# Kernel optimization log

Measured on AMD Instinct MI355X. Metric: run time of the kernel, lower is better.

Reference implementation:

```python
import jax, jax.numpy as jnp
import numpy as np

B, N = 2, 4096
SA, DG, ED, OUT = 128, 1024, 4, 128
RF = 0.1   # ED_radius_factor
EPS = 1e-5  # BatchNorm eps


def setup_inputs() -> dict:
    key = jax.random.key(0)
    ks = jax.random.split(key, 16)
    def w(k, sh, sc=0.05):
        return jax.random.normal(k, sh, jnp.float32) * sc
    return dict(
        pointcloud=jax.random.normal(ks[0], (B, N, 3), jnp.float32),
        h1=jax.random.normal(ks[1], (B, SA, N), jnp.float32),
        h2=jax.random.normal(ks[2], (B, DG, N), jnp.float32),
        dg_w1=w(ks[3], (256, DG)), dg_b1=jnp.zeros(256), dg_g1=jnp.ones(256), dg_be1=jnp.zeros(256),
        dg_w2=w(ks[4], (64, 256)), dg_b2=jnp.zeros(64), dg_g2=jnp.ones(64), dg_be2=jnp.zeros(64),
        dg_w3=w(ks[5], (32, 64)), dg_b3=jnp.zeros(32), dg_g3=jnp.ones(32), dg_be3=jnp.zeros(32),
        ed_w1=w(ks[6], (3, ED), 0.5), ed_b1=jnp.zeros(ED),
        ed_w2=w(ks[7], (ED, ED), 0.5), ed_b2=jnp.zeros(ED),
        w1=w(ks[8], (512, SA + 32 + ED)), b1=jnp.zeros(512), g1=jnp.ones(512), be1=jnp.zeros(512),
        w2=w(ks[9], (256, 512)), b2=jnp.zeros(256), g2=jnp.ones(256), be2=jnp.zeros(256),
        w3=w(ks[10], (OUT, 256)), b3=jnp.zeros(OUT), g3=jnp.ones(OUT), be3=jnp.zeros(OUT),
    )


def _conv1x1(x, w, b):  # x: (B,C,N) 1x1 Conv1d
    return jnp.einsum('oc,bcn->bon', w, x) + b[None, :, None]


def _bn(x, g, b):  # training-mode BatchNorm1d over (B,N) per channel
    m = x.mean(axis=(0, 2), keepdims=True)
    v = ((x - m) ** 2).mean(axis=(0, 2), keepdims=True)
    return g[None, :, None] * (x - m) * jax.lax.rsqrt(v + EPS) + b[None, :, None]


def _eigs(xyz):  # (N,3) -> (N,3) eigenvalues of per-point radius-neighbor covariance
    n = xyz.shape[0]
    x2 = (xyz * xyz).sum(-1)
    d2 = jnp.maximum(x2[:, None] + x2[None, :] - 2.0 * (xyz @ xyz.T), 0.0)
    dist = jnp.sqrt(jnp.maximum(d2, 1e-12))
    eye = jnp.eye(n, dtype=bool)
    max_d = jnp.where(eye, -jnp.inf, dist).max()  # calculate_distances max
    radius = max_d * RF                            # adaptive radius
    mask = ((dist < radius) & ~eye).astype(xyz.dtype)  # (N,N) radius neighbors, no self
    cnt = mask.sum(1)                              # true neighbor count (for the mean)
    mu = (mask @ xyz) / jnp.maximum(cnt, 1.0)[:, None]
    # sum_j m_ij x_j x_j^T via one matmul on flattened outer products
    S = (mask @ (xyz[:, :, None] * xyz[:, None, :]).reshape(n, 9)).reshape(n, 3, 3)
    # NOTE: original divides by k = mask.shape[0] == N (not neighbor count) -- kept faithfully
    cov = (S - cnt[:, None, None] * mu[:, :, None] * mu[:, None, :]) / n
    return jnp.linalg.eigvalsh(cov)


def reference(pointcloud, h1, h2,
              dg_w1, dg_b1, dg_g1, dg_be1,
              dg_w2, dg_b2, dg_g2, dg_be2,
              dg_w3, dg_b3, dg_g3, dg_be3,
              ed_w1, ed_b1, ed_w2, ed_b2,
              w1, b1, g1, be1, w2, b2, g2, be2, w3, b3, g3, be3):
    xyz = pointcloud[..., 0:3]
    # DG head: 1024 -> 256 -> 64 -> 32 (1x1 conv + BN + ReLU)
    f2 = jax.nn.relu(_bn(_conv1x1(h2, dg_w1, dg_b1), dg_g1, dg_be1))
    f2 = jax.nn.relu(_bn(_conv1x1(f2, dg_w2, dg_b2), dg_g2, dg_be2))
    f2 = jax.nn.relu(_bn(_conv1x1(f2, dg_w3, dg_b3), dg_g3, dg_be3))
    # ED branch: per-point local PCA eigenvalues + tiny MLP (3->4->4)
    eig = jax.vmap(_eigs)(xyz)                        # (B,N,3)
    h3 = jax.nn.relu(eig @ ed_w1 + ed_b1) @ ed_w2 + ed_b2  # (B,N,4)
    z = jnp.concatenate([h1, f2, jnp.transpose(h3, (0, 2, 1))], axis=1)  # (B,164,N)
    z = jax.nn.relu(_bn(_conv1x1(z, w1, b1), g1, be1))
    z = jax.nn.relu(_bn(_conv1x1(z, w2, b2), g2, be2))
    z = jax.nn.relu(_bn(_conv1x1(z, w3, b3), g3, be3))
    return (xyz, z)
```

## Files before the change

### kernel.cpp

```cpp
#include <hip/hip_runtime.h>
#include <math.h>

#define NPTS 4096
#define NB 2
#define BIGNEG -3.0e38f

typedef __attribute__((ext_vector_type(8))) short short8;
typedef __attribute__((ext_vector_type(4))) float f32x4;
typedef unsigned int uint32;

__device__ __forceinline__ unsigned short f2bf(float f) {
  uint32 u = __float_as_uint(f);
  uint32 r = (u + 0x7FFFu + ((u >> 16) & 1u)) >> 16;
  return (unsigned short)r;
}
__device__ __forceinline__ uint2 pack4(float a, float b, float c, float d) {
  uint2 r;
  r.x = (uint32)f2bf(a) | ((uint32)f2bf(b) << 16);
  r.y = (uint32)f2bf(c) | ((uint32)f2bf(d) << 16);
  return r;
}
__device__ __forceinline__ uint32 packtr(float lo, float hi) {
  return __builtin_amdgcn_perm(__float_as_uint(hi), __float_as_uint(lo), 0x07060302u);
}
__device__ __forceinline__ float bflo(uint32 w) { return __uint_as_float((w & 0xffffu) << 16); }
__device__ __forceinline__ float bfhi(uint32 w) { return __uint_as_float(w & 0xffff0000u); }

struct PrepP {
  const float *h2, *h1, *pc;
  const float* wsrc[6];
  unsigned short* wdst[6];
  unsigned short *h2t, *Zt;
  float *aZ, *bZ, *fZ, *f0;
  unsigned int* mx;
};

union ShPrep {
  float tile[64][65];
  struct { float4 sp[512]; float lm[8]; } m;
};

__global__ __launch_bounds__(256)
void prep_maxd2(PrepP P) {
  __shared__ ShPrep sh;
  int bid = blockIdx.x, tid = threadIdx.x;
  if (bid < 2304) {
    const float* src; unsigned short* dst; int S, C, b, c0, n0;
    if (bid < 2048) {
      b = bid >> 10; int r = bid & 1023;
      c0 = (r & 15) * 64; n0 = (r >> 4) * 64;
      src = P.h2; dst = P.h2t; S = 1024; C = 1024;
    } else {
      int r = bid - 2048; b = r >> 7; int r2 = r & 127;
      c0 = (r2 & 1) * 64; n0 = (r2 >> 1) * 64;
      src = P.h1; dst = P.Zt; S = 192; C = 128;
    }
    const float* sb = src + (size_t)b * C * NPTS;
#pragma unroll
    for (int p = 0; p < 4; ++p) {
      int r = (tid >> 4) + p * 16, q = tid & 15;
      float4 v = *(const float4*)(sb + (size_t)(c0 + r) * NPTS + n0 + q * 4);
      sh.tile[r][q * 4 + 0] = v.x;
      sh.tile[r][q * 4 + 1] = v.y;
      sh.tile[r][q * 4 + 2] = v.z;
      sh.tile[r][q * 4 + 3] = v.w;
    }
    __syncthreads();
#pragma unroll
    for (int p = 0; p < 2; ++p) {
      int n = (tid >> 3) + p * 32, j = tid & 7;
      uint2 lo = pack4(sh.tile[j * 8 + 0][n], sh.tile[j * 8 + 1][n], sh.tile[j * 8 + 2][n],
                       sh.tile[j * 8 + 3][n]);
      uint2 hi = pack4(sh.tile[j * 8 + 4][n], sh.tile[j * 8 + 5][n], sh.tile[j * 8 + 6][n],
                       sh.tile[j * 8 + 7][n]);
      *(uint4*)(dst + ((size_t)b * NPTS + n0 + n) * S + c0 + j * 8) =
          make_uint4(lo.x, lo.y, hi.x, hi.y);
    }
  } else if (bid < 2336) {
    int r = bid - 2304;
    for (int idx = r * 256 + tid; idx < NB * NPTS * 7; idx += 32 * 256) {
      int u = idx % 7, n = (idx / 7) & (NPTS - 1), b = idx / (7 * NPTS);
      *(uint2*)(P.Zt + ((size_t)b * NPTS + n) * 192 + 164 + u * 4) = make_uint2(0u, 0u);
    }
  } else if (bid < 2592) {
    const int segKp[6] = {1024, 256, 64, 192, 512, 256};
    const int segM[6] = {256, 64, 32, 512, 256, 128};
    const int segK[6] = {1024, 256, 64, 164, 512, 256};
    const int segEnd[6] = {262144, 278528, 282624, 380928, 512000, 544768};
    int r = bid - 2336;
    for (int idx = r * 256 + tid; idx < 544768; idx += 256 * 256) {
      int w = 0, start = 0;
#pragma unroll
      for (int s = 0; s < 6; ++s)
        if (idx >= segEnd[s]) { w = s + 1; start = segEnd[s]; }
      int local = idx - start, Kp = segKp[w], m = local / Kp, k = local % Kp;
      float v = (m < segM[w] && k < segK[w]) ? P.wsrc[w][m * segK[w] + k] : 0.f;
      P.wdst[w][local] = f2bf(v);
    }
  } else if (bid == 2592) {
    for (int ch = tid; ch < 512; ch += 256) {
      P.f0[ch] = 0.f;
      if (ch < 192) { P.aZ[ch] = 1.f; P.bZ[ch] = 0.f; P.fZ[ch] = BIGNEG; }
    }
  } else {
    int vb = bid - 2593;
    int b = vb >> 9, rem = vb & 511, it = rem & 63, jt = rem >> 6;
    int i0 = it * 64, j0 = jt * 512;
    const float* pb = P.pc + (size_t)b * NPTS * 3;
    for (int t = tid; t < 512; t += 256) {
      int j = j0 + t;
      float x = pb[j * 3], y = pb[j * 3 + 1], z = pb[j * 3 + 2];
      sh.m.sp[t] = make_float4(x, y, z, fmaf(x, x, fmaf(y, y, z * z)));
    }
    __syncthreads();
    int il = tid & 63, sl = tid >> 6;
    int i = i0 + il;
    float xi = pb[i * 3], yi = pb[i * 3 + 1], zi = pb[i * 3 + 2];
    float x2i = fmaf(xi, xi, fmaf(yi, yi, zi * zi));
    float m = 0.f;
#pragma unroll 4
    for (int j = sl * 128, e2 = sl * 128 + 128; j < e2; ++j) {
      float4 pj = sh.m.sp[j];
      float dot = fmaf(xi, pj.x, fmaf(yi, pj.y, zi * pj.z));
      m = fmaxf(m, fmaf(-2.f, dot, x2i + pj.w));
    }
#pragma unroll
    for (int off = 32; off > 0; off >>= 1) m = fmaxf(m, __shfl_xor(m, off, 64));
    if ((tid & 63) == 0) sh.m.lm[tid >> 6] = m;
    __syncthreads();
    if (tid == 0) {
      float v = fmaxf(fmaxf(sh.m.lm[0], sh.m.lm[1]), fmaxf(sh.m.lm[2], sh.m.lm[3]));
      atomicMax(&P.mx[b], __float_as_uint(v));
    }
  }
}

struct GemmP {
  const unsigned short* Wp;
  const unsigned short* X;
  const float *aIn, *bIn, *fIn;
  unsigned short* Y;
  int Ystride;
  float *psum, *psq;
  int M, Kp;
};
struct EigP {
  const float* pc;
  const unsigned int* mx;
  float* part;
  const float *ew1, *eb1, *ew2, *eb2;
  unsigned short* Zt;
};

union ShG {
  struct { char db[2][18432]; float ash[512], bsh[512], fsh[512]; } g;
  struct { float4 sp[1024]; float red[4][32][10]; } e;
};

template <int BN_IN, int EIG>
__global__ __launch_bounds__(256)
void gemm_k(GemmP P, EigP E) {
  __shared__ ShG sh;
  const int tid = threadIdx.x;

  if (EIG == 1 && blockIdx.z >= NB) {
    int e = blockIdx.x + 32 * blockIdx.y + 128 * (blockIdx.z - NB);
    int b = e >> 9, rem = e & 511, it = rem & 127, js = rem >> 7;
    int i0 = it * 32, j0 = js * 1024;
    const float* pb = E.pc + (size_t)b * NPTS * 3;
    for (int t = tid; t < 1024; t += 256) {
      int j = j0 + t;
      float x = pb[j * 3], y = pb[j * 3 + 1], z = pb[j * 3 + 2];
      sh.e.sp[t] = make_float4(x, y, z, fmaf(x, x, fmaf(y, y, z * z)));
    }
    __syncthreads();
    int il = tid & 31, sl = tid >> 5;
    int i = i0 + il;
    float xi = pb[i * 3], yi = pb[i * 3 + 1], zi = pb[i * 3 + 2];
    float x2i = fmaf(xi, xi, fmaf(yi, yi, zi * zi));
    float r2 = 0.01f * fmaxf(__uint_as_float(E.mx[b]), 1e-12f);
    float v0 = 0, v1 = 0, v2 = 0, v3 = 0, v4 = 0, v5 = 0, v6 = 0, v7 = 0, v8 = 0, v9 = 0;
#pragma unroll 2
    for (int j = sl * 128, e2 = sl * 128 + 128; j < e2; ++j) {
      float4 pj = sh.e.sp[j];
      float dot = fmaf(xi, pj.x, fmaf(yi, pj.y, zi * pj.z));
      float d2 = fmaf(-2.f, dot, x2i + pj.w);
      float msk = d2 < r2 ? 1.f : 0.f;
      float qx = msk * pj.x, qy = msk * pj.y, qz = msk * pj.z;
      v0 += msk; v1 += qx; v2 += qy; v3 += qz;
      v4 = fmaf(qx, pj.x, v4); v5 = fmaf(qx, pj.y, v5); v6 = fmaf(qx, pj.z, v6);
      v7 = fmaf(qy, pj.y, v7); v8 = fmaf(qy, pj.z, v8); v9 = fmaf(qz, pj.z, v9);
    }
    int iloc = i - j0;
    if (iloc >= sl * 128 && iloc < sl * 128 + 128) {
      v0 -= 1.f; v1 -= xi; v2 -= yi; v3 -= zi;
      v4 = fmaf(-xi, xi, v4); v5 = fmaf(-xi, yi, v5); v6 = fmaf(-xi, zi, v6);
      v7 = fmaf(-yi, yi, v7); v8 = fmaf(-yi, zi, v8); v9 = fmaf(-zi, zi, v9);
    }
    float vals[10] = {v0, v1, v2, v3, v4, v5, v6, v7, v8, v9};
#pragma unroll
    for (int v = 0; v < 10; ++v) vals[v] += __shfl_xor(vals[v], 32, 64);
    int w = tid >> 6;
    if ((tid & 63) < 32)
#pragma unroll
      for (int v = 0; v < 10; ++v) sh.e.red[w][il][v] = vals[v];
    __syncthreads();
    if (tid < 32) {
      int ii = i0 + tid;
      size_t base = ((size_t)(b * 4 + js) * 10) * NPTS + ii;
#pragma unroll
      for (int v = 0; v < 10; ++v)
        E.part[base + (size_t)v * NPTS] =
            sh.e.red[0][tid][v] + sh.e.red[1][tid][v] + sh.e.red[2][tid][v] +
            sh.e.red[3][tid][v];
    }
    return;
  }

  if (EIG == 2 && blockIdx.z >= NB) {
    int p = blockIdx.x * 256 + tid;
    int b = p >> 12, i = p & (NPTS - 1);
    float t[10];
#pragma unroll
    for (int v = 0; v < 10; ++v) {
      float s = 0.f;
#pragma unroll
      for (int js = 0; js < 4; ++js)
        s += E.part[((size_t)(b * 4 + js) * 10 + v) * NPTS + i];
      t[v] = s;
    }
    double cntd = (double)t[0];
    double denom = cntd > 1.0 ? cntd : 1.0;
    double mux = t[1] / denom, muy = t[2] / denom, muz = t[3] / denom;
    const double inv_n = 1.0 / (double)NPTS;
    double a00 = ((double)t[4] - cntd * mux * mux) * inv_n;
    double a01 = ((double)t[5] - cntd * mux * muy) * inv_n;
    double a02 = ((double)t[6] - cntd * mux * muz) * inv_n;
    double a11 = ((double)t[7] - cntd * muy * muy) * inv_n;
    double a12 = ((double)t[8] - cntd * muy * muz) * inv_n;
    double a22 = ((double)t[9] - cntd * muz * muz) * inv_n;
    double e0, e1, e2;
    double p1 = a01 * a01 + a02 * a02 + a12 * a12;
    double q = (a00 + a11 + a22) / 3.0;
    double d0 = a00 - q, d1 = a11 - q, d2q = a22 - q;
    double p2 = d0 * d0 + d1 * d1 + d2q * d2q + 2.0 * p1;
    if (p2 <= 1e-30) {
      e0 = e1 = e2 = q;
    } else {
      double pp = sqrt(p2 / 6.0);
      double ip = 1.0 / pp;
      double b00 = d0 * ip, b11 = d1 * ip, b22 = d2q * ip;
      double b01 = a01 * ip, b02 = a02 * ip, b12 = a12 * ip;
      double detB = b00 * (b11 * b22 - b12 * b12) - b01 * (b01 * b22 - b12 * b02) +
                    b02 * (b01 * b12 - b11 * b02);
      double r = detB * 0.5;
      r = r < -1.0 ? -1.0 : (r > 1.0 ? 1.0 : r);
      double phi = acos(r) / 3.0;
      e2 = q + 2.0 * pp * cos(phi);
      e0 = q + 2.0 * pp * cos(phi + 2.0943951023931953);
      e1 = 3.0 * q - e0 - e2;
    }
    float eg[3] = {(float)e0, (float)e1, (float)e2};
    float tmp[4];
#pragma unroll
    for (int e = 0; e < 4; ++e) {
      float v = E.eb1[e];
#pragma unroll
      for (int k = 0; k < 3; ++k) v = fmaf(eg[k], E.ew1[k * 4 + e], v);
      tmp[e] = fmaxf(v, 0.f);
    }
    float h3[4];
#pragma unroll
    for (int f = 0; f < 4; ++f) {
      float v = E.eb2[f];
#pragma unroll
      for (int e = 0; e < 4; ++e) v = fmaf(tmp[e], E.ew2[e * 4 + f], v);
      h3[f] = v;
    }
    *(uint2*)(E.Zt + ((size_t)b * NPTS + i) * 192 + 160) = pack4(h3[0], h3[1], h3[2], h3[3]);
    return;
  }

  const int b = blockIdx.z, nt = blockIdx.x, mt = blockIdx.y;
  const int n0 = nt * 128, m0 = mt * 64;
  const int lane = tid & 63, wid = tid >> 6;
  const int wm = wid >> 1, wn = wid & 1, g = lane >> 4, c = lane & 15;
  const int kt = P.Kp >> 6;
  const unsigned short* Xb = P.X + (size_t)b * NPTS * P.Kp;

  if (BN_IN) {
    for (int ch = tid; ch < P.Kp; ch += 256) {
      sh.g.ash[ch] = P.aIn[ch];
      sh.g.bsh[ch] = P.bIn[ch];
      sh.g.fsh[ch] = P.fIn[ch];
    }
    __syncthreads();
  }

  uint4 R0[4], R1[4];
  auto loadG = [&](int t, uint4* R) {
    int k0 = t << 6;
#pragma unroll
    for (int i = 0; i < 4; ++i) {
      int u = tid + i * 256, n = u >> 3, s = u & 7;
      R[i] = *(const uint4*)(Xb + (size_t)(n0 + n) * P.Kp + k0 + s * 8);
    }
  };
  auto writeS = [&](int buf, int t, uint4* R) {
    int k0 = t << 6;
#pragma unroll
    for (int i = 0; i < 4; ++i) {
      int u = tid + i * 256, s = u & 7;
      uint4 v = R[i];
      if (BN_IN) {
        int k = k0 + s * 8;
        float4 a0 = *(const float4*)&sh.g.ash[k], a1 = *(const float4*)&sh.g.ash[k + 4];
        float4 b0 = *(const float4*)&sh.g.bsh[k], b1 = *(const float4*)&sh.g.bsh[k + 4];
        float4 f0 = *(const float4*)&sh.g.fsh[k], f1 = *(const float4*)&sh.g.fsh[k + 4];
        float e0 = fmaxf(fmaf(bflo(v.x), a0.x, b0.x), f0.x);
        float e1 = fmaxf(fmaf(bfhi(v.x), a0.y, b0.y), f0.y);
        float e2 = fmaxf(fmaf(bflo(v.y), a0.z, b0.z), f0.z);
        float e3 = fmaxf(fmaf(bfhi(v.y), a0.w, b0.w), f0.w);
        float e4 = fmaxf(fmaf(bflo(v.z), a1.x, b1.x), f1.x);
        float e5 = fmaxf(fmaf(bfhi(v.z), a1.y, b1.y), f1.y);
        float e6 = fmaxf(fmaf(bflo(v.w), a1.z, b1.z), f1.z);
        float e7 = fmaxf(fmaf(bfhi(v.w), a1.w, b1.w), f1.w);
        v.x = packtr(e0, e1);
        v.y = packtr(e2, e3);
        v.z = packtr(e4, e5);
        v.w = packtr(e6, e7);
      }
      *(uint4*)&sh.g.db[buf][(u >> 3) * 144 + (u & 7) * 16] = v;
    }
  };
  auto loadA = [&](int t, uint4* Af) {
    const unsigned short* base = P.Wp + (size_t)(m0 + wm * 32 + c) * P.Kp + (t << 6) + g * 8;
#pragma unroll
    for (int mf = 0; mf < 2; ++mf)
#pragma unroll
      for (int kw = 0; kw < 2; ++kw)
        Af[mf * 2 + kw] = *(const uint4*)(base + (size_t)mf * 16 * P.Kp + kw * 32);
  };

  f32x4 acc[2][4] = {};
  uint4 Acur[4], Anext[4] = {};
  loadG(0, R0);
  loadA(0, Acur);
  writeS(0, 0, R0);
  if (kt > 1) loadG(1, R1);
  __syncthreads();
  int cur = 0;

  auto step = [&](int t, uint4* Rload, uint4* Rwrite) {
    if (t + 2 < kt) loadG(t + 2, Rload);
    if (t + 1 < kt) loadA(t + 1, Anext);
#pragma unroll
    for (int kw = 0; kw < 2; ++kw) {
      union { uint4 u; short8 s; } a0, a1;
      a0.u = Acur[0 * 2 + kw];
      a1.u = Acur[1 * 2 + kw];
#pragma unroll
      for (int nf = 0; nf < 4; ++nf) {
        union { uint4 u; short8 s; } bf;
        bf.u = *(const uint4*)&sh.g.db[cur][(wn * 64 + nf * 16 + c) * 144 + kw * 64 + g * 16];
        acc[0][nf] = __builtin_amdgcn_mfma_f32_16x16x32_bf16(a0.s, bf.s, acc[0][nf], 0, 0, 0);
        acc[1][nf] = __builtin_amdgcn_mfma_f32_16x16x32_bf16(a1.s, bf.s, acc[1][nf], 0, 0, 0);
      }
    }
    if (t + 1 < kt) writeS(cur ^ 1, t + 1, Rwrite);
    __syncthreads();
    cur ^= 1;
#pragma unroll
    for (int i = 0; i < 4; ++i) Acur[i] = Anext[i];
  };
  for (int t = 0; t < kt;) {
    step(t, R0, R1);
    ++t;
    if (t >= kt) break;
    step(t, R1, R0);
    ++t;
  }

#pragma unroll
  for (int nf = 0; nf < 4; ++nf) {
    int n = n0 + wn * 64 + nf * 16 + c;
    unsigned short* yrow = P.Y + ((size_t)b * NPTS + n) * P.Ystride;
#pragma unroll
    for (int mf = 0; mf < 2; ++mf) {
      int mb = m0 + wm * 32 + mf * 16 + g * 4;
      if (mb < P.M)
        *(uint2*)(yrow + mb) =
            pack4(acc[mf][nf][0], acc[mf][nf][1], acc[mf][nf][2], acc[mf][nf][3]);
    }
  }
  int slot = b * 64 + nt * 2 + wn;
#pragma unroll
  for (int mf = 0; mf < 2; ++mf)
#pragma unroll
    for (int r = 0; r < 4; ++r) {
      float s = 0.f, q = 0.f;
#pragma unroll
      for (int nf = 0; nf < 4; ++nf) {
        float v = acc[mf][nf][r];
        s += v;
        q = fmaf(v, v, q);
      }
#pragma unroll
      for (int m = 1; m < 16; m <<= 1) {
        s += __shfl_xor(s, m, 64);
        q += __shfl_xor(q, m, 64);
      }
      int row = m0 + wm * 32 + mf * 16 + g * 4 + r;
      if (c == 0 && row < P.M) {
        P.psum[(size_t)row * 128 + slot] = s;
        P.psq[(size_t)row * 128 + slot] = q;
      }
    }
}

__global__ __launch_bounds__(128)
void bn_finalize(const float* __restrict__ psum, const float* __restrict__ psq,
                 const float* __restrict__ gamma, const float* __restrict__ beta,
                 float* __restrict__ a_, float* __restrict__ b_, float* __restrict__ f_) {
  int ch = blockIdx.x, t = threadIdx.x;
  float s = psum[(size_t)ch * 128 + t];
  float q = psq[(size_t)ch * 128 + t];
#pragma unroll
  for (int m = 1; m < 64; m <<= 1) {
    s += __shfl_xor(s, m, 64);
    q += __shfl_xor(q, m, 64);
  }
  __shared__ float ws[2][2];
  if ((t & 63) == 0) { ws[t >> 6][0] = s; ws[t >> 6][1] = q; }
  __syncthreads();
  if (t == 0) {
    float S = ws[0][0] + ws[1][0];
    float Q = ws[0][1] + ws[1][1];
    const float inv = 1.f / (float)(NB * NPTS);
    float mean = S * inv;
    float var = fmaxf(Q * inv - mean * mean, 0.f);
    float aa = rsqrtf(var + 1e-5f) * gamma[ch];
    a_[ch] = aa;
    b_[ch] = beta[ch] - mean * aa;
    if (f_) f_[ch] = 0.f;
  }
}

__global__ __launch_bounds__(256)
void out_final(const unsigned short* __restrict__ Y, const float* __restrict__ a_,
               const float* __restrict__ b_, const float* __restrict__ pc,
               float* __restrict__ out) {
  int bid = blockIdx.x;
  if (bid < 1024) {
    __shared__ float tile[32][33];
    int b = bid >> 9, r0 = bid & 511;
    int c0 = (r0 & 3) * 32, n0 = (r0 >> 2) * 32;
    int r = threadIdx.x >> 3, q = threadIdx.x & 7;
    uint2 v = *(const uint2*)(Y + ((size_t)b * NPTS + n0 + r) * 128 + c0 + q * 4);
    float4 aa = *(const float4*)(a_ + c0 + q * 4);
    float4 bb = *(const float4*)(b_ + c0 + q * 4);
    tile[r][q * 4 + 0] = fmaxf(bflo(v.x) * aa.x + bb.x, 0.f);
    tile[r][q * 4 + 1] = fmaxf(bfhi(v.x) * aa.y + bb.y, 0.f);
    tile[r][q * 4 + 2] = fmaxf(bflo(v.y) * aa.z + bb.z, 0.f);
    tile[r][q * 4 + 3] = fmaxf(bfhi(v.y) * aa.w + bb.w, 0.f);
    __syncthreads();
    float4 o = make_float4(tile[q * 4 + 0][r], tile[q * 4 + 1][r], tile[q * 4 + 2][r],
                           tile[q * 4 + 3][r]);
    float* z = out + (size_t)NB * NPTS * 3;
    *(float4*)(z + ((size_t)b * 128 + c0 + r) * NPTS + n0 + q * 4) = o;
  } else {
    int i = (bid - 1024) * 256 + threadIdx.x;
    ((float4*)out)[i] = ((const float4*)pc)[i];
  }
}

extern "C" void kernel_launch(void* const* d_in, const int* in_sizes, int n_in,
                              void* d_out, int out_size, void* d_ws, size_t ws_size,
                              hipStream_t stream) {
  (void)in_sizes; (void)n_in; (void)out_size; (void)ws_size;
  const float* pc    = (const float*)d_in[0];
  const float* h1    = (const float*)d_in[1];
  const float* h2    = (const float*)d_in[2];
  const float* dgw1  = (const float*)d_in[3];
  const float* dgg1  = (const float*)d_in[5];
  const float* dgbe1 = (const float*)d_in[6];
  const float* dgw2  = (const float*)d_in[7];
  const float* dgg2  = (const float*)d_in[9];
  const float* dgbe2 = (const float*)d_in[10];
  const float* dgw3  = (const float*)d_in[11];
  const float* dgg3  = (const float*)d_in[13];
  const float* dgbe3 = (const float*)d_in[14];
  const float* ew1   = (const float*)d_in[15];
  const float* eb1   = (const float*)d_in[16];
  const float* ew2   = (const float*)d_in[17];
  const float* eb2   = (const float*)d_in[18];
  const float* w1    = (const float*)d_in[19];
  const float* g1    = (const float*)d_in[21];
  const float* be1   = (const float*)d_in[22];
  const float* w2    = (const float*)d_in[23];
  const float* g2    = (const float*)d_in[25];
  const float* be2   = (const float*)d_in[26];
  const float* w3    = (const float*)d_in[27];
  const float* g3    = (const float*)d_in[29];
  const float* be3   = (const float*)d_in[30];
  float* out = (float*)d_out;

  char* p = (char*)d_ws;
  auto take = [&](size_t bytes) { char* r = p; p += (bytes + 255) & ~(size_t)255; return r; };
  unsigned int* mx = (unsigned int*)take(64);
  unsigned short* h2t = (unsigned short*)take((size_t)NB * NPTS * 1024 * 2);
  unsigned short* Zt  = (unsigned short*)take((size_t)NB * NPTS * 192 * 2);
  unsigned short* wp1 = (unsigned short*)take((size_t)256 * 1024 * 2);
  unsigned short* wp2 = (unsigned short*)take((size_t)64 * 256 * 2);
  unsigned short* wp3 = (unsigned short*)take((size_t)64 * 64 * 2);
  unsigned short* wp4 = (unsigned short*)take((size_t)512 * 192 * 2);
  unsigned short* wp5 = (unsigned short*)take((size_t)256 * 512 * 2);
  unsigned short* wp6 = (unsigned short*)take((size_t)128 * 256 * 2);
  unsigned short* yA  = (unsigned short*)take((size_t)NB * NPTS * 256 * 2);
  unsigned short* yB  = (unsigned short*)take((size_t)NB * NPTS * 512 * 2);
  float* psum = (float*)take((size_t)512 * 128 * 4);
  float* psq  = (float*)take((size_t)512 * 128 * 4);
  float* a1 = (float*)take(512 * 4); float* b1 = (float*)take(512 * 4);
  float* a2 = (float*)take(512 * 4); float* b2 = (float*)take(512 * 4);
  float* aZ = (float*)take(512 * 4); float* bZ = (float*)take(512 * 4);
  float* fZ = (float*)take(512 * 4);
  float* a4 = (float*)take(512 * 4); float* b4 = (float*)take(512 * 4);
  float* a5 = (float*)take(512 * 4); float* b5 = (float*)take(512 * 4);
  float* a6 = (float*)take(512 * 4); float* b6 = (float*)take(512 * 4);
  float* f0 = (float*)take(512 * 4);
  float* part = (float*)take((size_t)NB * 4 * 10 * NPTS * 4);

  hipMemsetAsync(mx, 0, 64, stream);

  PrepP PP;
  PP.h2 = h2; PP.h1 = h1; PP.pc = pc;
  PP.wsrc[0] = dgw1; PP.wsrc[1] = dgw2; PP.wsrc[2] = dgw3;
  PP.wsrc[3] = w1;   PP.wsrc[4] = w2;   PP.wsrc[5] = w3;
  PP.wdst[0] = wp1; PP.wdst[1] = wp2; PP.wdst[2] = wp3;
  PP.wdst[3] = wp4; PP.wdst[4] = wp5; PP.wdst[5] = wp6;
  PP.h2t = h2t; PP.Zt = Zt;
  PP.aZ = aZ; PP.bZ = bZ; PP.fZ = fZ; PP.f0 = f0;
  PP.mx = mx;
  prep_maxd2<<<3617, 256, 0, stream>>>(PP);

  EigP EP = {pc, mx, part, ew1, eb1, ew2, eb2, Zt};

  GemmP L1 = {wp1, h2t, nullptr, nullptr, nullptr, yA, 256, psum, psq, 256, 1024};
  gemm_k<0, 1><<<dim3(32, 4, NB + 8), 256, 0, stream>>>(L1, EP);
  bn_finalize<<<256, 128, 0, stream>>>(psum, psq, dgg1, dgbe1, a1, b1, nullptr);

  GemmP L2 = {wp2, yA, a1, b1, f0, yB, 64, psum, psq, 64, 256};
  gemm_k<1, 2><<<dim3(32, 1, NB + 1), 256, 0, stream>>>(L2, EP);
  bn_finalize<<<64, 128, 0, stream>>>(psum, psq, dgg2, dgbe2, a2, b2, nullptr);

  GemmP L3 = {wp3, yB, a2, b2, f0, Zt + 128, 192, psum, psq, 32, 64};
  gemm_k<1, 0><<<dim3(32, 1, NB), 256, 0, stream>>>(L3, EP);
  bn_finalize<<<32, 128, 0, stream>>>(psum, psq, dgg3, dgbe3, aZ + 128, bZ + 128, fZ + 128);

  GemmP L4 = {wp4, Zt, aZ, bZ, fZ, yB, 512, psum, psq, 512, 192};
  gemm_k<1, 0><<<dim3(32, 8, NB), 256, 0, stream>>>(L4, EP);
  bn_finalize<<<512, 128, 0, stream>>>(psum, psq, g1, be1, a4, b4, nullptr);

  GemmP L5 = {wp5, yB, a4, b4, f0, yA, 256, psum, psq, 256, 512};
  gemm_k<1, 0><<<dim3(32, 4, NB), 256, 0, stream>>>(L5, EP);
  bn_finalize<<<256, 128, 0, stream>>>(psum, psq, g2, be2, a5, b5, nullptr);

  GemmP L6 = {wp6, yA, a5, b5, f0, yB, 128, psum, psq, 128, 256};
  gemm_k<1, 0><<<dim3(32, 2, NB), 256, 0, stream>>>(L6, EP);
  bn_finalize<<<128, 128, 0, stream>>>(psum, psq, g3, be3, a6, b6, nullptr);

  out_final<<<1048, 256, 0, stream>>>(yB, a6, b6, pc, out);
}
```

Baseline: 140.5 us.

## Fuse BatchNorm finalize into the prologue of each following GEMM

```diff
diff --git a/kernel.cpp b/kernel.cpp
--- a/kernel.cpp
+++ b/kernel.cpp
@@ -31,7 +31,6 @@
   const float* wsrc[6];
   unsigned short* wdst[6];
   unsigned short *h2t, *Zt;
-  float *aZ, *bZ, *fZ, *f0;
   unsigned int* mx;
 };
 
@@ -97,13 +96,8 @@
       float v = (m < segM[w] && k < segK[w]) ? P.wsrc[w][m * segK[w] + k] : 0.f;
       P.wdst[w][local] = f2bf(v);
     }
-  } else if (bid == 2592) {
-    for (int ch = tid; ch < 512; ch += 256) {
-      P.f0[ch] = 0.f;
-      if (ch < 192) { P.aZ[ch] = 1.f; P.bZ[ch] = 0.f; P.fZ[ch] = BIGNEG; }
-    }
   } else {
-    int vb = bid - 2593;
+    int vb = bid - 2592;
     int b = vb >> 9, rem = vb & 511, it = rem & 63, jt = rem >> 6;
     int i0 = it * 64, j0 = jt * 512;
     const float* pb = P.pc + (size_t)b * NPTS * 3;
@@ -138,10 +132,11 @@
 struct GemmP {
   const unsigned short* Wp;
   const unsigned short* X;
-  const float *aIn, *bIn, *fIn;
+  const float *psIn, *pqIn, *gam, *bet;
+  int chOff, nch;
   unsigned short* Y;
   int Ystride;
-  float *psum, *psq;
+  float *psO, *pqO;
   int M, Kp;
 };
 struct EigP {
@@ -290,9 +285,30 @@
 
   if (BN_IN) {
     for (int ch = tid; ch < P.Kp; ch += 256) {
-      sh.g.ash[ch] = P.aIn[ch];
-      sh.g.bsh[ch] = P.bIn[ch];
-      sh.g.fsh[ch] = P.fIn[ch];
+      sh.g.ash[ch] = 1.f;
+      sh.g.bsh[ch] = 0.f;
+      sh.g.fsh[ch] = BIGNEG;
+    }
+    __syncthreads();
+    for (int idx = tid; idx < P.nch; idx += 256) {
+      const float4* s4 = (const float4*)(P.psIn + (size_t)idx * 128);
+      const float4* q4 = (const float4*)(P.pqIn + (size_t)idx * 128);
+      float s = 0.f, q = 0.f;
+#pragma unroll 8
+      for (int i = 0; i < 32; ++i) {
+        float4 a = s4[i];
+        s += a.x + a.y + a.z + a.w;
+        float4 w = q4[i];
+        q += w.x + w.y + w.z + w.w;
+      }
+      const float inv = 1.f / 8192.f;
+      float mean = s * inv;
+      float var = fmaxf(q * inv - mean * mean, 0.f);
+      float aa = rsqrtf(var + 1e-5f) * P.gam[idx];
+      int ch = P.chOff + idx;
+      sh.g.ash[ch] = aa;
+      sh.g.bsh[ch] = P.bet[idx] - mean * aa;
+      sh.g.fsh[ch] = 0.f;
     }
     __syncthreads();
   }
@@ -412,8 +428,8 @@
       }
       int row = m0 + wm * 32 + mf * 16 + g * 4 + r;
       if (c == 0 && row < P.M) {
-        P.psum[(size_t)row * 128 + slot] = s;
-        P.psq[(size_t)row * 128 + slot] = q;
+        P.psO[(size_t)row * 128 + slot] = s;
+        P.pqO[(size_t)row * 128 + slot] = q;
       }
     }
 }
@@ -421,7 +437,7 @@
 __global__ __launch_bounds__(128)
 void bn_finalize(const float* __restrict__ psum, const float* __restrict__ psq,
                  const float* __restrict__ gamma, const float* __restrict__ beta,
-                 float* __restrict__ a_, float* __restrict__ b_, float* __restrict__ f_) {
+                 float* __restrict__ a_, float* __restrict__ b_) {
   int ch = blockIdx.x, t = threadIdx.x;
   float s = psum[(size_t)ch * 128 + t];
   float q = psq[(size_t)ch * 128 + t];
@@ -442,7 +458,6 @@
     float aa = rsqrtf(var + 1e-5f) * gamma[ch];
     a_[ch] = aa;
     b_[ch] = beta[ch] - mean * aa;
-    if (f_) f_[ch] = 0.f;
   }
 }
 
@@ -518,16 +533,12 @@
   unsigned short* wp6 = (unsigned short*)take((size_t)128 * 256 * 2);
   unsigned short* yA  = (unsigned short*)take((size_t)NB * NPTS * 256 * 2);
   unsigned short* yB  = (unsigned short*)take((size_t)NB * NPTS * 512 * 2);
-  float* psum = (float*)take((size_t)512 * 128 * 4);
-  float* psq  = (float*)take((size_t)512 * 128 * 4);
-  float* a1 = (float*)take(512 * 4); float* b1 = (float*)take(512 * 4);
-  float* a2 = (float*)take(512 * 4); float* b2 = (float*)take(512 * 4);
-  float* aZ = (float*)take(512 * 4); float* bZ = (float*)take(512 * 4);
-  float* fZ = (float*)take(512 * 4);
-  float* a4 = (float*)take(512 * 4); float* b4 = (float*)take(512 * 4);
-  float* a5 = (float*)take(512 * 4); float* b5 = (float*)take(512 * 4);
-  float* a6 = (float*)take(512 * 4); float* b6 = (float*)take(512 * 4);
-  float* f0 = (float*)take(512 * 4);
+  float* psA = (float*)take((size_t)512 * 128 * 4);
+  float* pqA = (float*)take((size_t)512 * 128 * 4);
+  float* psB = (float*)take((size_t)512 * 128 * 4);
+  float* pqB = (float*)take((size_t)512 * 128 * 4);
+  float* a6 = (float*)take(512 * 4);
+  float* b6 = (float*)take(512 * 4);
   float* part = (float*)take((size_t)NB * 4 * 10 * NPTS * 4);
 
   hipMemsetAsync(mx, 0, 64, stream);
@@ -539,35 +550,35 @@
   PP.wdst[0] = wp1; PP.wdst[1] = wp2; PP.wdst[2] = wp3;
   PP.wdst[3] = wp4; PP.wdst[4] = wp5; PP.wdst[5] = wp6;
   PP.h2t = h2t; PP.Zt = Zt;
-  PP.aZ = aZ; PP.bZ = bZ; PP.fZ = fZ; PP.f0 = f0;
   PP.mx = mx;
-  prep_maxd2<<<3617, 256, 0, stream>>>(PP);
+  prep_maxd2<<<3616, 256, 0, stream>>>(PP);
 
   EigP EP = {pc, mx, part, ew1, eb1, ew2, eb2, Zt};
 
-  GemmP L1 = {wp1, h2t, nullptr, nullptr, nullptr, yA, 256, psum, psq, 256, 1024};
+  GemmP L1 = {wp1, h2t, nullptr, nullptr, nullptr, nullptr, 0, 0,
+              yA, 256, psA, pqA, 256, 1024};
   gemm_k<0, 1><<<dim3(32, 4, NB + 8), 256, 0, stream>>>(L1, EP);
-  bn_finalize<<<256, 128, 0, stream>>>(psum, psq, dgg1, dgbe1, a1, b1, nullptr);
-
-  GemmP L2 = {wp2, yA, a1, b1, f0, yB, 64, psum, psq, 64, 256};
+
+  GemmP L2 = {wp2, yA, psA, pqA, dgg1, dgbe1, 0, 256,
+              yB, 64, psB, pqB, 64, 256};
   gemm_k<1, 2><<<dim3(32, 1, NB + 1), 256, 0, stream>>>(L2, EP);
-  bn_finalize<<<64, 128, 0, stream>>>(psum, psq, dgg2, dgbe2, a2, b2, nullptr);
-
-  GemmP L3 = {wp3, yB, a2, b2, f0, Zt + 128, 192, psum, psq, 32, 64};
+
+  GemmP L3 = {wp3, yB, psB, pqB, dgg2, dgbe2, 0, 64,
+              Zt + 128, 192, psA, pqA, 32, 64};
   gemm_k<1, 0><<<dim3(32, 1, NB), 256, 0, stream>>>(L3, EP);
-  bn_finalize<<<32, 128, 0, stream>>>(psum, psq, dgg3, dgbe3, aZ + 128, bZ + 128, fZ + 128);
-
-  GemmP L4 = {wp4, Zt, aZ, bZ, fZ, yB, 512, psum, psq, 512, 192};
+
+  GemmP L4 = {wp4, Zt, psA, pqA, dgg3, dgbe3, 128, 32,
+              yB, 512, psB, pqB, 512, 192};
   gemm_k<1, 0><<<dim3(32, 8, NB), 256, 0, stream>>>(L4, EP);
-  bn_finalize<<<512, 128, 0, stream>>>(psum, psq, g1, be1, a4, b4, nullptr);
-
-  GemmP L5 = {wp5, yB, a4, b4, f0, yA, 256, psum, psq, 256, 512};
+
+  GemmP L5 = {wp5, yB, psB, pqB, g1, be1, 0, 512,
+              yA, 256, psA, pqA, 256, 512};
   gemm_k<1, 0><<<dim3(32, 4, NB), 256, 0, stream>>>(L5, EP);
-  bn_finalize<<<256, 128, 0, stream>>>(psum, psq, g2, be2, a5, b5, nullptr);
-
-  GemmP L6 = {wp6, yA, a5, b5, f0, yB, 128, psum, psq, 128, 256};
+
+  GemmP L6 = {wp6, yA, psA, pqA, g2, be2, 0, 256,
+              yB, 128, psB, pqB, 128, 256};
   gemm_k<1, 0><<<dim3(32, 2, NB), 256, 0, stream>>>(L6, EP);
-  bn_finalize<<<128, 128, 0, stream>>>(psum, psq, g3, be3, a6, b6, nullptr);
-
+
+  bn_finalize<<<128, 128, 0, stream>>>(psB, pqB, g3, be3, a6, b6);
   out_final<<<1048, 256, 0, stream>>>(yB, a6, b6, pc, out);
 }
```

Result: slower. 164.7 us (+17.2%).
